# Kernel optimization log

Hardware: AMD Instinct MI355X
Metric: run time of the kernel (lower is better)

The kernel has to match this reference:

```python
import jax, jax.numpy as jnp
import numpy as np
from jax import lax

WINDOW_SIZE = 11
SIGMA = 1.5
C1 = 0.01 ** 2
C2 = 0.03 ** 2


def _make_window():
    xs = np.arange(WINDOW_SIZE) - WINDOW_SIZE // 2
    g = np.exp(-(xs.astype(np.float32) ** 2) / (2.0 * SIGMA ** 2))
    g = g / g.sum()
    w2d = np.outer(g, g).astype(np.float32)  # (ws, ws)
    return jnp.asarray(w2d)[None, None, :, :]  # (O=1, I=1, ws, ws)


def _blur(x, window):
    pad = WINDOW_SIZE // 2
    return lax.conv_general_dilated(
        x, window,
        window_strides=(1, 1),
        padding=[(pad, pad), (pad, pad)],
        dimension_numbers=("NCHW", "OIHW", "NCHW"),
    )


def setup_inputs() -> dict:
    key = jax.random.key(0)
    k1, k2 = jax.random.split(key)
    shape = (64, 1, 512, 512)
    img1 = jax.random.uniform(k1, shape, dtype=jnp.float32)
    img2 = jax.random.uniform(k2, shape, dtype=jnp.float32)
    return {"img1": img1, "img2": img2}


def reference(img1, img2):
    window = _make_window()
    mu1 = _blur(img1, window)
    mu2 = _blur(img2, window)
    mu1_sq = mu1 * mu1
    mu2_sq = mu2 * mu2
    mu1_mu2 = mu1 * mu2
    sigma1_sq = _blur(img1 * img1, window) - mu1_sq
    sigma2_sq = _blur(img2 * img2, window) - mu2_sq
    sigma12 = _blur(img1 * img2, window) - mu1_mu2
    ssim_map = ((2.0 * mu1_mu2 + C1) * (2.0 * sigma12 + C2)) / (
        (mu1_sq + mu2_sq + C1) * (sigma1_sq + sigma2_sq + C2)
    )
    return ssim_map.mean()  # size_average=True
```

## Files before the change

### kernel.cpp

```cpp
#include <hip/hip_runtime.h>

#define IMG 512
#define HALO 5
#define BAND 16
#define NB 16
#define RING 28

#define W0 1.0283800e-03f
#define W1 7.5987582e-03f
#define W2 3.6000773e-02f
#define W3 1.0936070e-01f
#define W4 2.1300553e-01f
#define W5 2.6601172e-01f

typedef float f2 __attribute__((ext_vector_type(2)));

__device__ __forceinline__ f2 pkfma(f2 a, f2 b, f2 c) {
    return __builtin_elementwise_fma(a, b, c);
}

#define LGKM_BARRIER() asm volatile("s_waitcnt lgkmcnt(0)\n\ts_barrier" ::: "memory")

__global__ __launch_bounds__(256, 4)
void ssim_main(const float* __restrict__ img1, const float* __restrict__ img2,
               float* __restrict__ part)
{
    const float Wt[11] = {W0,W1,W2,W3,W4,W5,W4,W3,W2,W1,W0};
    constexpr float C1 = 1.0e-4f;
    constexpr float C2 = 9.0e-4f;

    __shared__ float4 sH[RING][65];
    __shared__ float  sRed[4];

    const int bx     = blockIdx.x;
    const int n      = bx >> 4;
    const int stripe = (bx >> 1) & 7;
    const int half   = bx & 1;
    const int gx0    = stripe << 6;
    const int base   = half << 8;
    const int tid    = threadIdx.x;
    const bool edge  = (stripe == 0) | (stripe == 7);

    const float* __restrict__ base1 = img1 + (size_t)n * IMG * IMG;
    const float* __restrict__ base2 = img2 + (size_t)n * IMG * IMG;

    float acc = 0.0f;

    auto loadRowP = [&](const float* r1, const float* r2, bool rok, int gcb,
                        float4* px, float4* py) {
        #pragma unroll
        for (int t = 0; t < 5; ++t) {
            int gc = gcb - 8 + (t << 2);
            bool ok = rok && (gc >= 0) && (gc < IMG);
            px[t] = ok ? ((const float4*)r1)[t] : make_float4(0.f,0.f,0.f,0.f);
            py[t] = ok ? ((const float4*)r2)[t] : make_float4(0.f,0.f,0.f,0.f);
        }
    };

    auto horizStore = [&](const float4* px, const float4* py, int slot, int cg) {
        const int c0 = cg << 2;
        float X[20], Y[20];
        #pragma unroll
        for (int t = 0; t < 5; ++t) {
            X[4*t+0]=px[t].x; X[4*t+1]=px[t].y; X[4*t+2]=px[t].z; X[4*t+3]=px[t].w;
            Y[4*t+0]=py[t].x; Y[4*t+1]=py[t].y; Y[4*t+2]=py[t].z; Y[4*t+3]=py[t].w;
        }
        f2 xy[14], sp[14];
        #pragma unroll
        for (int j = 0; j < 14; ++j) {
            float x = X[3+j], y = Y[3+j];
            xy[j] = f2{x, y};
            sp[j] = f2{fmaf(x, x, y*y), x*y};
        }
        #pragma unroll
        for (int o = 0; o < 4; ++o) {
            f2 m = {0.f, 0.f}, t2 = {0.f, 0.f};
            #pragma unroll
            for (int k = 0; k < 11; ++k) {
                f2 w2 = {Wt[k], Wt[k]};
                m  = pkfma(w2, xy[o+k], m);
                t2 = pkfma(w2, sp[o+k], t2);
            }
            sH[slot][c0+o] = make_float4(m.x, m.y, t2.x, t2.y);
        }
    };

    for (int task = tid; task < 26 * 16; task += 256) {
        int i   = task >> 4;
        int cg  = task & 15;
        int gr  = base - HALO + i;
        int gcb = gx0 + (cg << 2);
        const float* r1 = base1 + (ptrdiff_t)gr * IMG + gcb - 8;
        const float* r2 = base2 + (ptrdiff_t)gr * IMG + gcb - 8;
        float4 px[5], py[5];
        loadRowP(r1, r2, (unsigned)gr < (unsigned)IMG, gcb, px, py);
        horizStore(px, py, i, cg);
    }

    const int rr  = tid >> 4;
    const int cgs = tid & 15;
    const int gcb = gx0 + (cgs << 2);
    const float* p1 = base1 + (ptrdiff_t)(base + 21 + rr) * IMG + gcb - 8;
    const float* p2 = base2 + (ptrdiff_t)(base + 21 + rr) * IMG + gcb - 8;

    int sb = 0;
    for (int b = 0; b < NB; ++b) {
        float4 px[5], py[5];
        const bool pf = (b + 1 < NB);
        if (pf) {
            const bool rowsafe = (half == 0) | (b < 14);
            if (rowsafe & (!edge)) {
                #pragma unroll
                for (int t = 0; t < 5; ++t) {
                    px[t] = ((const float4*)p1)[t];
                    py[t] = ((const float4*)p2)[t];
                }
            } else {
                int gr = base + (b << 4) + 21 + rr;
                loadRowP(p1, p2, (unsigned)gr < (unsigned)IMG, gcb, px, py);
            }
        }

        LGKM_BARRIER();

        {
            const int wv  = __builtin_amdgcn_readfirstlane(tid >> 6);
            const int col = tid & 63;
            const int d0  = sb + (wv << 2);
            f2 a[14], p[14];
            #pragma unroll
            for (int i = 0; i < 14; ++i) {
                int s = d0 + i;
                s -= (s >= RING) ? RING : 0;
                s -= (s >= RING) ? RING : 0;
                float4 q = sH[s][col];
                a[i] = f2{q.x, q.y};
                p[i] = f2{q.z, q.w};
            }
            #pragma unroll
            for (int q4 = 0; q4 < 4; ++q4) {
                f2 m = {0.f,0.f}, tt = {0.f,0.f};
                #pragma unroll
                for (int k = 0; k < 11; ++k) {
                    f2 w2 = {Wt[k], Wt[k]};
                    m  = pkfma(w2, a[q4+k], m);
                    tt = pkfma(w2, p[q4+k], tt);
                }
                f2 msq     = m * m;
                float mu12  = m.x * m.y;
                float musum = msq.x + msq.y;
                float g12   = tt.y - mu12;
                float gs    = tt.x - musum;
                float num = fmaf(2.f, mu12, C1) * fmaf(2.f, g12, C2);
                float den = (musum + C1) * (gs + C2);
                acc = fmaf(num, __builtin_amdgcn_rcpf(den), acc);
            }
        }

        LGKM_BARRIER();

        if (pf) {
            int t = sb + 26 + rr;
            t -= (t >= RING) ? RING : 0;
            t -= (t >= RING) ? RING : 0;
            horizStore(px, py, t, cgs);
            p1 += BAND * IMG;
            p2 += BAND * IMG;
        }
        sb += BAND;
        sb -= (sb >= RING) ? RING : 0;
    }

    #pragma unroll
    for (int off = 32; off > 0; off >>= 1)
        acc += __shfl_down(acc, off, 64);
    if ((tid & 63) == 0) sRed[tid >> 6] = acc;
    LGKM_BARRIER();
    if (tid == 0) part[bx] = sRed[0] + sRed[1] + sRed[2] + sRed[3];
}

__global__ void ssim_finalize(const float* __restrict__ part, float* __restrict__ out)
{
    double s = 0.0;
    const int t = threadIdx.x;
    for (int i = t; i < 1024; i += 64) s += (double)part[i];
    #pragma unroll
    for (int off = 32; off > 0; off >>= 1)
        s += __shfl_down(s, off, 64);
    if (t == 0) out[0] = (float)(s * (1.0 / 16777216.0));
}

extern "C" void kernel_launch(void* const* d_in, const int* in_sizes, int n_in,
                              void* d_out, int out_size, void* d_ws, size_t ws_size,
                              hipStream_t stream)
{
    const float* img1 = (const float*)d_in[0];
    const float* img2 = (const float*)d_in[1];
    float* out  = (float*)d_out;
    float* part = (float*)d_ws;

    ssim_main<<<1024, 256, 0, stream>>>(img1, img2, part);
    ssim_finalize<<<1, 64, 0, stream>>>(part, out);
}
```

Baseline: 174.6 us.

## Store horizontal blur intermediates as fp16 in a 64-row ring, split rows into quarters

The horizontal-pass results (mu1, mu2, x²+y², xy) now go into shared memory packed as fp16 pairs instead of float4. The ring grows to 64 slots indexed by masked row number, so only one barrier per band is needed instead of two. The grid doubles to 2048 blocks, each covering a quarter of the rows. This halves LDS traffic and footprint and adds parallelism, but fp16 storage of the second moments risks precision loss in the variance subtraction, and the extra blocks recompute more halo rows.

```diff
diff --git a/kernel.cpp b/kernel.cpp
--- a/kernel.cpp
+++ b/kernel.cpp
@@ -1,18 +1,17 @@
 #include <hip/hip_runtime.h>
 
 #define IMG 512
-#define HALO 5
-#define BAND 16
-#define NB 16
-#define RING 28
-
-#define W0 1.0283800e-03f
-#define W1 7.5987582e-03f
-#define W2 3.6000773e-02f
-#define W3 1.0936070e-01f
-#define W4 2.1300553e-01f
-#define W5 2.6601172e-01f
-
+#define NB 8
+
+#define W0f 1.0283800e-03f
+#define W1f 7.5987582e-03f
+#define W2f 3.6000773e-02f
+#define W3f 1.0936070e-01f
+#define W4f 2.1300553e-01f
+#define W5f 2.6601172e-01f
+
+typedef _Float16 h1;
+typedef h1 h2 __attribute__((ext_vector_type(2)));
 typedef float f2 __attribute__((ext_vector_type(2)));
 
 __device__ __forceinline__ f2 pkfma(f2 a, f2 b, f2 c) {
@@ -25,165 +24,169 @@
 void ssim_main(const float* __restrict__ img1, const float* __restrict__ img2,
                float* __restrict__ part)
 {
-    const float Wt[11] = {W0,W1,W2,W3,W4,W5,W4,W3,W2,W1,W0};
-    constexpr float C1 = 1.0e-4f;
-    constexpr float C2 = 9.0e-4f;
-
-    __shared__ float4 sH[RING][65];
-    __shared__ float  sRed[4];
+    __shared__ float4 ringRaw[64 * 32];
+    float2* const rp2 = (float2*)ringRaw;
+
+    const float Wt[11] = {W0f,W1f,W2f,W3f,W4f,W5f,W4f,W3f,W2f,W1f,W0f};
+    constexpr float C1 = 1.0e-4f, C2 = 9.0e-4f;
 
     const int bx     = blockIdx.x;
-    const int n      = bx >> 4;
-    const int stripe = (bx >> 1) & 7;
-    const int half   = bx & 1;
+    const int n      = bx >> 5;
+    const int stripe = (bx >> 2) & 7;
+    const int q      = bx & 3;
     const int gx0    = stripe << 6;
-    const int base   = half << 8;
+    const int base   = q << 7;
     const int tid    = threadIdx.x;
     const bool edge  = (stripe == 0) | (stripe == 7);
 
-    const float* __restrict__ base1 = img1 + (size_t)n * IMG * IMG;
-    const float* __restrict__ base2 = img2 + (size_t)n * IMG * IMG;
-
-    float acc = 0.0f;
-
-    auto loadRowP = [&](const float* r1, const float* r2, bool rok, int gcb,
-                        float4* px, float4* py) {
+    const float* __restrict__ b1p = img1 + (size_t)n * IMG * IMG;
+    const float* __restrict__ b2p = img2 + (size_t)n * IMG * IMG;
+
+    float acc = 0.f;
+
+    auto loadRow = [&](int gr, int gcb, float4* PX, float4* PY) {
+        const float* r1 = b1p + (ptrdiff_t)gr * IMG + (gcb - 8);
+        const float* r2 = b2p + (ptrdiff_t)gr * IMG + (gcb - 8);
+        const bool rok = (unsigned)gr < (unsigned)IMG;
+        if (rok & (!edge)) {
+            #pragma unroll
+            for (int t = 0; t < 5; ++t) {
+                PX[t] = ((const float4*)r1)[t];
+                PY[t] = ((const float4*)r2)[t];
+            }
+        } else {
+            #pragma unroll
+            for (int t = 0; t < 5; ++t) {
+                int gc = gcb - 8 + (t << 2);
+                bool ok = rok && (gc >= 0) && (gc <= IMG - 4);
+                PX[t] = ok ? ((const float4*)r1)[t] : make_float4(0.f,0.f,0.f,0.f);
+                PY[t] = ok ? ((const float4*)r2)[t] : make_float4(0.f,0.f,0.f,0.f);
+            }
+        }
+    };
+
+    auto horizStore = [&](int gr, int cg, const float4* PX, const float4* PY) {
+        float X[20], Y[20];
         #pragma unroll
         for (int t = 0; t < 5; ++t) {
-            int gc = gcb - 8 + (t << 2);
-            bool ok = rok && (gc >= 0) && (gc < IMG);
-            px[t] = ok ? ((const float4*)r1)[t] : make_float4(0.f,0.f,0.f,0.f);
-            py[t] = ok ? ((const float4*)r2)[t] : make_float4(0.f,0.f,0.f,0.f);
-        }
-    };
-
-    auto horizStore = [&](const float4* px, const float4* py, int slot, int cg) {
-        const int c0 = cg << 2;
-        float X[20], Y[20];
-        #pragma unroll
-        for (int t = 0; t < 5; ++t) {
-            X[4*t+0]=px[t].x; X[4*t+1]=px[t].y; X[4*t+2]=px[t].z; X[4*t+3]=px[t].w;
-            Y[4*t+0]=py[t].x; Y[4*t+1]=py[t].y; Y[4*t+2]=py[t].z; Y[4*t+3]=py[t].w;
-        }
-        f2 xy[14], sp[14];
+            X[4*t]=PX[t].x; X[4*t+1]=PX[t].y; X[4*t+2]=PX[t].z; X[4*t+3]=PX[t].w;
+            Y[4*t]=PY[t].x; Y[4*t+1]=PY[t].y; Y[4*t+2]=PY[t].z; Y[4*t+3]=PY[t].w;
+        }
+        f2 pxy[14], psp[14];
         #pragma unroll
         for (int j = 0; j < 14; ++j) {
             float x = X[3+j], y = Y[3+j];
-            xy[j] = f2{x, y};
-            sp[j] = f2{fmaf(x, x, y*y), x*y};
-        }
+            pxy[j] = f2{x, y};
+            psp[j] = f2{fmaf(x, x, y*y), x*y};
+        }
+        f2 axy[4], asp[4];
         #pragma unroll
         for (int o = 0; o < 4; ++o) {
-            f2 m = {0.f, 0.f}, t2 = {0.f, 0.f};
+            f2 m = {0.f,0.f}, t2 = {0.f,0.f};
             #pragma unroll
             for (int k = 0; k < 11; ++k) {
                 f2 w2 = {Wt[k], Wt[k]};
-                m  = pkfma(w2, xy[o+k], m);
-                t2 = pkfma(w2, sp[o+k], t2);
-            }
-            sH[slot][c0+o] = make_float4(m.x, m.y, t2.x, t2.y);
+                m  = pkfma(w2, pxy[o+k], m);
+                t2 = pkfma(w2, psp[o+k], t2);
+            }
+            axy[o] = m; asp[o] = t2;
+        }
+        const int slot = (gr + 64) & 63;
+        float4* dst = ringRaw + (slot << 5) + (cg << 1);
+        #pragma unroll
+        for (int pp = 0; pp < 2; ++pp) {
+            float4 st;
+            h2 a0 = h2{(h1)axy[2*pp].x,   (h1)axy[2*pp].y};
+            h2 b0 = h2{(h1)asp[2*pp].x,   (h1)asp[2*pp].y};
+            h2 a1 = h2{(h1)axy[2*pp+1].x, (h1)axy[2*pp+1].y};
+            h2 b1 = h2{(h1)asp[2*pp+1].x, (h1)asp[2*pp+1].y};
+            st.x = __builtin_bit_cast(float, a0);
+            st.y = __builtin_bit_cast(float, b0);
+            st.z = __builtin_bit_cast(float, a1);
+            st.w = __builtin_bit_cast(float, b1);
+            dst[pp] = st;
         }
     };
 
-    for (int task = tid; task < 26 * 16; task += 256) {
-        int i   = task >> 4;
-        int cg  = task & 15;
-        int gr  = base - HALO + i;
-        int gcb = gx0 + (cg << 2);
-        const float* r1 = base1 + (ptrdiff_t)gr * IMG + gcb - 8;
-        const float* r2 = base2 + (ptrdiff_t)gr * IMG + gcb - 8;
-        float4 px[5], py[5];
-        loadRowP(r1, r2, (unsigned)gr < (unsigned)IMG, gcb, px, py);
-        horizStore(px, py, i, cg);
+    auto vert = [&](int b) {
+        const int wv  = __builtin_amdgcn_readfirstlane(tid >> 6);
+        const int col = tid & 63;
+        const int gr0 = base + (b << 4) + (wv << 2) - 5 + 64;
+        h2 vxy[14], vsp[14];
+        #pragma unroll
+        for (int i = 0; i < 14; ++i) {
+            const int slot = (gr0 + i) & 63;
+            float2 qv = rp2[(slot << 6) + col];
+            vxy[i] = __builtin_bit_cast(h2, qv.x);
+            vsp[i] = __builtin_bit_cast(h2, qv.y);
+        }
+        #pragma unroll
+        for (int qd = 0; qd < 4; ++qd) {
+            float m1=0.f, m2=0.f, ts=0.f, tp=0.f;
+            #pragma unroll
+            for (int k = 0; k < 11; ++k) {
+                const float w = Wt[k];
+                m1 = fmaf((float)vxy[qd+k].x, w, m1);
+                m2 = fmaf((float)vxy[qd+k].y, w, m2);
+                ts = fmaf((float)vsp[qd+k].x, w, ts);
+                tp = fmaf((float)vsp[qd+k].y, w, tp);
+            }
+            float mu12  = m1 * m2;
+            float musum = fmaf(m1, m1, m2*m2);
+            float g12 = tp - mu12;
+            float gs  = ts - musum;
+            float num = fmaf(2.f, mu12, C1) * fmaf(2.f, g12, C2);
+            float den = (musum + C1) * (gs + C2);
+            acc = fmaf(num, __builtin_amdgcn_rcpf(den), acc);
+        }
+    };
+
+    const int ri  = tid >> 4;
+    const int cg  = tid & 15;
+    const int gcb = gx0 + (cg << 2);
+
+    {
+        float4 PX[5], PY[5];
+        int gr = base - 5 + ri;
+        loadRow(gr, gcb, PX, PY);
+        horizStore(gr, cg, PX, PY);
+        int task = tid + 256;
+        if (task < 26 * 16) {
+            int gr2 = base - 5 + (task >> 4);
+            int cg2 = task & 15;
+            loadRow(gr2, gx0 + (cg2 << 2), PX, PY);
+            horizStore(gr2, cg2, PX, PY);
+        }
     }
 
-    const int rr  = tid >> 4;
-    const int cgs = tid & 15;
-    const int gcb = gx0 + (cgs << 2);
-    const float* p1 = base1 + (ptrdiff_t)(base + 21 + rr) * IMG + gcb - 8;
-    const float* p2 = base2 + (ptrdiff_t)(base + 21 + rr) * IMG + gcb - 8;
-
-    int sb = 0;
+    float4 PX[5], PY[5];
+    loadRow(base + 21 + ri, gcb, PX, PY);
+
     for (int b = 0; b < NB; ++b) {
-        float4 px[5], py[5];
-        const bool pf = (b + 1 < NB);
-        if (pf) {
-            const bool rowsafe = (half == 0) | (b < 14);
-            if (rowsafe & (!edge)) {
-                #pragma unroll
-                for (int t = 0; t < 5; ++t) {
-                    px[t] = ((const float4*)p1)[t];
-                    py[t] = ((const float4*)p2)[t];
-                }
-            } else {
-                int gr = base + (b << 4) + 21 + rr;
-                loadRowP(p1, p2, (unsigned)gr < (unsigned)IMG, gcb, px, py);
-            }
-        }
-
+        const int r0 = base + (b << 4);
         LGKM_BARRIER();
-
-        {
-            const int wv  = __builtin_amdgcn_readfirstlane(tid >> 6);
-            const int col = tid & 63;
-            const int d0  = sb + (wv << 2);
-            f2 a[14], p[14];
-            #pragma unroll
-            for (int i = 0; i < 14; ++i) {
-                int s = d0 + i;
-                s -= (s >= RING) ? RING : 0;
-                s -= (s >= RING) ? RING : 0;
-                float4 q = sH[s][col];
-                a[i] = f2{q.x, q.y};
-                p[i] = f2{q.z, q.w};
-            }
-            #pragma unroll
-            for (int q4 = 0; q4 < 4; ++q4) {
-                f2 m = {0.f,0.f}, tt = {0.f,0.f};
-                #pragma unroll
-                for (int k = 0; k < 11; ++k) {
-                    f2 w2 = {Wt[k], Wt[k]};
-                    m  = pkfma(w2, a[q4+k], m);
-                    tt = pkfma(w2, p[q4+k], tt);
-                }
-                f2 msq     = m * m;
-                float mu12  = m.x * m.y;
-                float musum = msq.x + msq.y;
-                float g12   = tt.y - mu12;
-                float gs    = tt.x - musum;
-                float num = fmaf(2.f, mu12, C1) * fmaf(2.f, g12, C2);
-                float den = (musum + C1) * (gs + C2);
-                acc = fmaf(num, __builtin_amdgcn_rcpf(den), acc);
-            }
-        }
-
-        LGKM_BARRIER();
-
-        if (pf) {
-            int t = sb + 26 + rr;
-            t -= (t >= RING) ? RING : 0;
-            t -= (t >= RING) ? RING : 0;
-            horizStore(px, py, t, cgs);
-            p1 += BAND * IMG;
-            p2 += BAND * IMG;
-        }
-        sb += BAND;
-        sb -= (sb >= RING) ? RING : 0;
+        if (b < NB-1) horizStore(r0 + 21 + ri, cg, PX, PY);
+        if (b < NB-2) loadRow(r0 + 37 + ri, gcb, PX, PY);
+        vert(b);
     }
 
     #pragma unroll
     for (int off = 32; off > 0; off >>= 1)
         acc += __shfl_down(acc, off, 64);
-    if ((tid & 63) == 0) sRed[tid >> 6] = acc;
     LGKM_BARRIER();
-    if (tid == 0) part[bx] = sRed[0] + sRed[1] + sRed[2] + sRed[3];
+    if ((tid & 63) == 0) ((float*)ringRaw)[tid >> 6] = acc;
+    LGKM_BARRIER();
+    if (tid == 0) {
+        const float* r = (const float*)ringRaw;
+        part[bx] = r[0] + r[1] + r[2] + r[3];
+    }
 }
 
 __global__ void ssim_finalize(const float* __restrict__ part, float* __restrict__ out)
 {
     double s = 0.0;
     const int t = threadIdx.x;
-    for (int i = t; i < 1024; i += 64) s += (double)part[i];
+    for (int i = t; i < 2048; i += 64) s += (double)part[i];
     #pragma unroll
     for (int off = 32; off > 0; off >>= 1)
         s += __shfl_down(s, off, 64);
@@ -199,6 +202,6 @@
     float* out  = (float*)d_out;
     float* part = (float*)d_ws;
 
-    ssim_main<<<1024, 256, 0, stream>>>(img1, img2, part);
+    ssim_main<<<2048, 256, 0, stream>>>(img1, img2, part);
     ssim_finalize<<<1, 64, 0, stream>>>(part, out);
 }
```

Measured after the change: 180.9 us. 1.04x slower.
